# Kernel tuning notes

Hardware: AMD Instinct MI355X
Metric: run time of the kernel (lower is better)

Reference implementation:

```python
import jax, jax.numpy as jnp
import numpy as np

HID = 512
J = 64
NEG = -1e9


def _gru_cell(x, h, Wih, Whh, bih, bhh):
    # PyTorch GRUCell: gates stacked as (r, z, n) along first dim of (3H, in)
    gi = Wih @ x + bih          # (3H,)
    gh = Whh @ h + bhh          # (3H,)
    r = jax.nn.sigmoid(gi[:HID] + gh[:HID])
    z = jax.nn.sigmoid(gi[HID:2 * HID] + gh[HID:2 * HID])
    n = jnp.tanh(gi[2 * HID:] + r * gh[2 * HID:])
    return (1.0 - z) * n + z * h


def setup_inputs() -> dict:
    key = jax.random.key(0)
    ks = jax.random.split(key, 8)
    T = 4096
    state_dim = 2 * J  # input is state[t][1:]
    d = {
        "state": jax.random.normal(ks[0], (T, state_dim + 1), dtype=jnp.float32),
        "h_prev": jnp.zeros((2, HID), dtype=jnp.float32),
        "mask": jax.random.randint(ks[1], (J, J), 0, 2, dtype=jnp.int32),
        "Wih0": jax.random.normal(ks[2], (3 * HID, state_dim), dtype=jnp.float32) * 0.05,
        "Whh0": jax.random.normal(ks[3], (3 * HID, HID), dtype=jnp.float32) * 0.04,
        "bih0": jnp.zeros((3 * HID,), dtype=jnp.float32),
        "bhh0": jnp.zeros((3 * HID,), dtype=jnp.float32),
        "Wih1": jax.random.normal(ks[4], (3 * HID, HID), dtype=jnp.float32) * 0.04,
        "Whh1": jax.random.normal(ks[5], (3 * HID, HID), dtype=jnp.float32) * 0.04,
        "bih1": jnp.zeros((3 * HID,), dtype=jnp.float32),
        "bhh1": jnp.zeros((3 * HID,), dtype=jnp.float32),
        "Wfc": jax.random.normal(ks[6], (J * J, HID), dtype=jnp.float32) * 0.06,
        "bfc": jnp.zeros((J * J,), dtype=jnp.float32),
    }
    return d


def reference(state, h_prev, mask, Wih0, Whh0, bih0, bhh0,
              Wih1, Whh1, bih1, bhh1, Wfc, bfc):
    xs = state[:, 1:]  # drop leading element, matches state[t][1:]

    def step(hs, x_t):
        h0 = _gru_cell(x_t, hs[0], Wih0, Whh0, bih0, bhh0)
        h1 = _gru_cell(h0, hs[1], Wih1, Whh1, bih1, bhh1)
        new = jnp.stack([h0, h1])
        return new, h1

    h_next, h_list = jax.lax.scan(step, h_prev, xs)  # h_list: (T, HID)
    logits = jax.nn.relu(h_list @ Wfc.T + bfc)       # (T, J*J)
    logits = logits.reshape(-1, J, J)
    logits = jnp.where(mask == 0, jnp.float32(NEG), logits)
    return logits, h_next
```

## Files before the change

### kernel.cpp

```cpp
#include <hip/hip_runtime.h>
#include <stdint.h>

#define TSTEPS   4096
#define NEG_VAL  -1000000000.0f
#define NWG_SCAN 96
#define G0WG     32
#define RINGN    32

#define GI0_OFF   0
#define H1_OFF    (TSTEPS*1536*4)
#define RING0_OFF (H1_OFF + TSTEPS*512*4)
#define RING1_OFF (RING0_OFF + RINGN*512*8)
#define ARR_OFF   (RING1_OFF + RINGN*512*8)
#define WS_NEED   ((size_t)ARR_OFF + RINGN*64)

static __device__ __forceinline__ unsigned long long ld_a64(const unsigned long long* p){
  return __hip_atomic_load(p, __ATOMIC_RELAXED, __HIP_MEMORY_SCOPE_AGENT);
}
static __device__ __forceinline__ void st_a64(unsigned long long* p, unsigned long long v){
  __hip_atomic_store(p, v, __ATOMIC_RELAXED, __HIP_MEMORY_SCOPE_AGENT);
}
static __device__ __forceinline__ float sigmoidf_(float x){
  return 1.0f / (1.0f + __expf(-x));
}
static __device__ __forceinline__ float tanhf_(float x){
  float ax = fabsf(x);
  float e  = __expf(-2.0f*ax);
  float t  = (1.0f - e) / (1.0f + e);
  return copysignf(t, x);
}

static __device__ __forceinline__ void spin_to_lds(const unsigned long long* ring, int slot,
                                                   unsigned want, int lane, float* dst,
                                                   long* budget){
  const unsigned long long* bp = ring + (size_t)slot*512 + lane;
  unsigned long long v[8];
  for(;;){
    #pragma unroll
    for (int j=0;j<8;++j) v[j] = ld_a64(bp + j*64);
    bool ok = true;
    #pragma unroll
    for (int j=0;j<8;++j) ok = ok && ((unsigned)(v[j]>>32) == want);
    if (ok) break;
    if (--(*budget) < 0) break;
  }
  #pragma unroll
  for (int j=0;j<8;++j) dst[j*64+lane] = __uint_as_float((unsigned)v[j]);
}

__global__ __launch_bounds__(384,1) void gru_scan(
    const float* __restrict__ gi0,
    const float* __restrict__ hprev,
    const float* __restrict__ Whh0,
    const float* __restrict__ Wih1,
    const float* __restrict__ Whh1,
    const float* __restrict__ bhh0,
    const float* __restrict__ bih1,
    const float* __restrict__ bhh1,
    float* __restrict__ H1hist,
    unsigned long long* ring0,
    unsigned long long* ring1,
    unsigned* arr,
    float* __restrict__ hnext)
{
  const int wg   = blockIdx.x;
  const int tid  = threadIdx.x;
  const int wave = tid >> 6;
  const int lane = tid & 63;

  __shared__ float hbuf0[512];
  __shared__ float hbuf1[512];
  __shared__ float sc[64];

  long budget = (1L<<22);

  if (wg < G0WG) {
    const int ibase = wg*16;
    float w[8][8];
    #pragma unroll
    for (int k=0;k<8;++k){
      const int rid = wave*8+k;
      const int g = rid>>4, il = rid&15;
      const float* wp = Whh0 + ((size_t)(g*512 + ibase + il))*512;
      #pragma unroll
      for (int j=0;j<8;++j) w[k][j] = wp[j*64 + lane];
    }
    float hreg=0.f, br=0.f, bz=0.f, bn_=0.f;
    const int mi = ibase + tid;
    if (tid < 16){
      hreg = hprev[mi];
      br  = bhh0[mi]; bz = bhh0[512+mi]; bn_ = bhh0[1024+mi];
    }
    for (int t=0; t<TSTEPS; ++t){
      float gr=0.f, gz=0.f, gn=0.f;
      if (tid < 16){
        const float* gp = gi0 + (size_t)t*1536 + mi;
        gr = gp[0]; gz = gp[512]; gn = gp[1024];
      }
      if (wave == 0){
        if (t == 0){
          #pragma unroll
          for (int j=0;j<8;++j) hbuf0[j*64+lane] = hprev[j*64+lane];
        } else {
          spin_to_lds(ring0, (t-1)&(RINGN-1), (unsigned)t, lane, hbuf0, &budget);
        }
      }
      if (tid==0 && t>=16){
        unsigned* ap = arr + (size_t)((t-16)&(RINGN-1))*16;
        const unsigned expect = (unsigned)NWG_SCAN * (unsigned)(((t-16)>>5)+1);
        while (__hip_atomic_load(ap, __ATOMIC_RELAXED, __HIP_MEMORY_SCOPE_AGENT) < expect){
          if (--budget < 0) break;
        }
      }
      __syncthreads();
      float hj[8];
      #pragma unroll
      for (int j=0;j<8;++j) hj[j] = hbuf0[j*64+lane];
      float acc[8];
      #pragma unroll
      for (int k=0;k<8;++k){
        float a = 0.f;
        #pragma unroll
        for (int j=0;j<8;++j) a = fmaf(w[k][j], hj[j], a);
        #pragma unroll
        for (int off=32; off; off>>=1) a += __shfl_xor(a, off, 64);
        acc[k] = a;
      }
      if (lane == 0){
        #pragma unroll
        for (int k=0;k<8;++k) sc[wave*8+k] = acc[k];
      }
      __syncthreads();
      if (tid < 16){
        const float ghr = sc[tid]    + br;
        const float ghz = sc[16+tid] + bz;
        const float ghn = sc[32+tid] + bn_;
        const float r = sigmoidf_(gr + ghr);
        const float z = sigmoidf_(gz + ghz);
        const float n = tanhf_(gn + r*ghn);
        const float h = (1.f - z)*n + z*hreg;
        hreg = h;
        st_a64(ring0 + (size_t)(t&(RINGN-1))*512 + mi,
               ((unsigned long long)(unsigned)(t+1)<<32) |
               (unsigned long long)__float_as_uint(h));
        if (t == TSTEPS-1) hnext[mi] = h;
      }
      __syncthreads();
      if (tid == 0){
        __hip_atomic_fetch_add(arr + (size_t)(t&(RINGN-1))*16, 1u,
                               __ATOMIC_RELEASE, __HIP_MEMORY_SCOPE_AGENT);
      }
    }
  } else {
    const int wgl = wg - G0WG;
    const int ibase = wgl*8;
    const bool isA = (wave < 3);
    float w[8][8];
    #pragma unroll
    for (int k=0;k<8;++k){
      const int rid = (isA ? wave : (wave-3))*8 + k;
      const int g = rid>>3, il = rid&7;
      const float* W = isA ? Wih1 : Whh1;
      const float* wp = W + ((size_t)(g*512 + ibase + il))*512;
      #pragma unroll
      for (int j=0;j<8;++j) w[k][j] = wp[j*64 + lane];
    }
    float hreg=0.f, bir=0.f,biz=0.f,bin_=0.f, bhr=0.f,bhz=0.f,bhn=0.f;
    const int mi = ibase + tid;
    if (tid < 8){
      hreg = hprev[512+mi];
      bir = bih1[mi]; biz = bih1[512+mi]; bin_ = bih1[1024+mi];
      bhr = bhh1[mi]; bhz = bhh1[512+mi]; bhn  = bhh1[1024+mi];
    }
    for (int s=0; s<TSTEPS; ++s){
      if (wave == 0){
        spin_to_lds(ring0, s&(RINGN-1), (unsigned)(s+1), lane, hbuf0, &budget);
      } else if (wave == 3){
        if (s == 0){
          #pragma unroll
          for (int j=0;j<8;++j) hbuf1[j*64+lane] = hprev[512 + j*64+lane];
        } else {
          spin_to_lds(ring1, (s-1)&(RINGN-1), (unsigned)s, lane, hbuf1, &budget);
        }
      }
      if (tid==0 && s>=16){
        unsigned* ap = arr + (size_t)((s-16)&(RINGN-1))*16;
        const unsigned expect = (unsigned)NWG_SCAN * (unsigned)(((s-16)>>5)+1);
        while (__hip_atomic_load(ap, __ATOMIC_RELAXED, __HIP_MEMORY_SCOPE_AGENT) < expect){
          if (--budget < 0) break;
        }
      }
      __syncthreads();
      const float* hsrc = isA ? hbuf0 : hbuf1;
      float hj[8];
      #pragma unroll
      for (int j=0;j<8;++j) hj[j] = hsrc[j*64+lane];
      float acc[8];
      #pragma unroll
      for (int k=0;k<8;++k){
        float a = 0.f;
        #pragma unroll
        for (int j=0;j<8;++j) a = fmaf(w[k][j], hj[j], a);
        #pragma unroll
        for (int off=32; off; off>>=1) a += __shfl_xor(a, off, 64);
        acc[k] = a;
      }
      if (lane == 0){
        const int base = isA ? (wave*8) : (24 + (wave-3)*8);
        #pragma unroll
        for (int k=0;k<8;++k) sc[base+k] = acc[k];
      }
      __syncthreads();
      if (tid < 8){
        const float gir = sc[tid]    + bir;
        const float giz = sc[8+tid]  + biz;
        const float gin = sc[16+tid] + bin_;
        const float ghr = sc[24+tid] + bhr;
        const float ghz = sc[32+tid] + bhz;
        const float ghn = sc[40+tid] + bhn;
        const float r = sigmoidf_(gir + ghr);
        const float z = sigmoidf_(giz + ghz);
        const float n = tanhf_(gin + r*ghn);
        const float h = (1.f - z)*n + z*hreg;
        hreg = h;
        st_a64(ring1 + (size_t)(s&(RINGN-1))*512 + mi,
               ((unsigned long long)(unsigned)(s+1)<<32) |
               (unsigned long long)__float_as_uint(h));
        H1hist[(size_t)s*512 + mi] = h;
        if (s == TSTEPS-1) hnext[512+mi] = h;
      }
      __syncthreads();
      if (tid == 0){
        __hip_atomic_fetch_add(arr + (size_t)(s&(RINGN-1))*16, 1u,
                               __ATOMIC_RELEASE, __HIP_MEMORY_SCOPE_AGENT);
      }
    }
  }
}

template<int EPI>
__global__ __launch_bounds__(256) void gemm_nt(
    const float* __restrict__ A, int lda,
    const float* __restrict__ B, int ldb,
    float* __restrict__ C, int ldc,
    const float* __restrict__ bias,
    const int* __restrict__ mask,
    int K)
{
  __shared__ __align__(16) float As[32][68];
  __shared__ __align__(16) float Bs[32][68];
  const int bm = blockIdx.y*64, bn = blockIdx.x*64;
  const int tid = threadIdx.x;
  const int tm = tid>>4, tn = tid&15;
  float acc[4][4] = {};
  const int m0 = tid>>2, kk0 = (tid&3)*8;
  for (int k0=0; k0<K; k0+=32){
    #pragma unroll
    for (int j=0;j<8;++j) As[kk0+j][m0] = A[(size_t)(bm+m0)*lda + k0+kk0+j];
    #pragma unroll
    for (int j=0;j<8;++j) Bs[kk0+j][m0] = B[(size_t)(bn+m0)*ldb + k0+kk0+j];
    __syncthreads();
    #pragma unroll
    for (int kk=0;kk<32;++kk){
      const float4 av = *(const float4*)&As[kk][tm*4];
      const float4 bv = *(const float4*)&Bs[kk][tn*4];
      acc[0][0]=fmaf(av.x,bv.x,acc[0][0]); acc[0][1]=fmaf(av.x,bv.y,acc[0][1]);
      acc[0][2]=fmaf(av.x,bv.z,acc[0][2]); acc[0][3]=fmaf(av.x,bv.w,acc[0][3]);
      acc[1][0]=fmaf(av.y,bv.x,acc[1][0]); acc[1][1]=fmaf(av.y,bv.y,acc[1][1]);
      acc[1][2]=fmaf(av.y,bv.z,acc[1][2]); acc[1][3]=fmaf(av.y,bv.w,acc[1][3]);
      acc[2][0]=fmaf(av.z,bv.x,acc[2][0]); acc[2][1]=fmaf(av.z,bv.y,acc[2][1]);
      acc[2][2]=fmaf(av.z,bv.z,acc[2][2]); acc[2][3]=fmaf(av.z,bv.w,acc[2][3]);
      acc[3][0]=fmaf(av.w,bv.x,acc[3][0]); acc[3][1]=fmaf(av.w,bv.y,acc[3][1]);
      acc[3][2]=fmaf(av.w,bv.z,acc[3][2]); acc[3][3]=fmaf(av.w,bv.w,acc[3][3]);
    }
    __syncthreads();
  }
  #pragma unroll
  for (int i=0;i<4;++i){
    #pragma unroll
    for (int j=0;j<4;++j){
      const int mm = bm + tm*4 + i, cc = bn + tn*4 + j;
      float v = acc[i][j] + bias[cc];
      if (EPI){
        v = fmaxf(v, 0.f);
        if (mask[cc] == 0) v = NEG_VAL;
      }
      C[(size_t)mm*ldc + cc] = v;
    }
  }
}

extern "C" void kernel_launch(void* const* d_in, const int* in_sizes, int n_in,
                              void* d_out, int out_size, void* d_ws, size_t ws_size,
                              hipStream_t stream)
{
  const float* state = (const float*)d_in[0];
  const float* hprev = (const float*)d_in[1];
  const int*   mask  = (const int*)d_in[2];
  const float* Wih0  = (const float*)d_in[3];
  const float* Whh0  = (const float*)d_in[4];
  const float* bih0  = (const float*)d_in[5];
  const float* bhh0  = (const float*)d_in[6];
  const float* Wih1  = (const float*)d_in[7];
  const float* Whh1  = (const float*)d_in[8];
  const float* bih1  = (const float*)d_in[9];
  const float* bhh1  = (const float*)d_in[10];
  const float* Wfc   = (const float*)d_in[11];
  const float* bfc   = (const float*)d_in[12];

  if (ws_size < WS_NEED) return;

  float* out = (float*)d_out;
  char*  ws  = (char*)d_ws;
  float* gi0 = (float*)(ws + GI0_OFF);
  float* H1  = (float*)(ws + H1_OFF);
  unsigned long long* ring0 = (unsigned long long*)(ws + RING0_OFF);
  unsigned long long* ring1 = (unsigned long long*)(ws + RING1_OFF);
  unsigned* arr = (unsigned*)(ws + ARR_OFF);

  (void)hipMemsetAsync(ws + RING0_OFF, 0, (size_t)(WS_NEED - RING0_OFF), stream);

  {
    dim3 grid(1536/64, 4096/64);
    gemm_nt<0><<<grid, 256, 0, stream>>>(state+1, 129, Wih0, 128, gi0, 1536,
                                         bih0, nullptr, 128);
  }

  gru_scan<<<NWG_SCAN, 384, 0, stream>>>(gi0, hprev, Whh0, Wih1, Whh1,
                                         bhh0, bih1, bhh1,
                                         H1, ring0, ring1, arr,
                                         out + (size_t)4096*4096);

  {
    dim3 grid(4096/64, 4096/64);
    gemm_nt<1><<<grid, 256, 0, stream>>>(H1, 512, Wfc, 512, out, 4096,
                                         bfc, mask, 512);
  }
}
```

Before: 12.84 ms.

## Fuse GRU scan with FC GEMM in persistent kernel using fp16 dot2 recurrences

Replaces the scan kernel and the separate FC GEMM with one persistent kernel. Eight workgroups run the layer-0 recurrence, eight run the layer-1 hidden recurrence, and eight compute the layer-1 input projection as a separate pipeline stage. The remaining workgroups take FC GEMM tiles from a ticket counter as H1 rows become ready, so the output GEMM overlaps the serial scan. Weights are held in registers as fp16, and hidden states are exchanged as packed fp16 through small rings with per-slot tags and fdot2, which cuts per-step latency and traffic. The cost is lower precision in the recurrent matvecs and a more complex cross-workgroup synchronisation scheme that can deadlock.

```diff
diff --git a/kernel.cpp b/kernel.cpp
--- a/kernel.cpp
+++ b/kernel.cpp
@@ -1,23 +1,35 @@
 #include <hip/hip_runtime.h>
 #include <stdint.h>
 
-#define TSTEPS   4096
-#define NEG_VAL  -1000000000.0f
-#define NWG_SCAN 96
-#define G0WG     32
-#define RINGN    32
-
-#define GI0_OFF   0
-#define H1_OFF    (TSTEPS*1536*4)
-#define RING0_OFF (H1_OFF + TSTEPS*512*4)
-#define RING1_OFF (RING0_OFF + RINGN*512*8)
-#define ARR_OFF   (RING1_OFF + RINGN*512*8)
-#define WS_NEED   ((size_t)ARR_OFF + RINGN*64)
-
-static __device__ __forceinline__ unsigned long long ld_a64(const unsigned long long* p){
+#define TS 4096
+#define NEG_VAL -1000000000.0f
+
+typedef _Float16 h2 __attribute__((ext_vector_type(2)));
+typedef unsigned long long u64t;
+
+#define GI0_OFF   ((size_t)0)
+#define H1_OFF    ((size_t)TS*1536*4)
+#define R0_OFF    (H1_OFF + (size_t)TS*512*4)
+#define R1_OFF    (R0_OFF + (size_t)16*128*8)
+#define GIR_OFF   (R1_OFF + (size_t)16*128*8)
+#define TAG0_OFF  (GIR_OFF + (size_t)16*1536*4)
+#define TAG1_OFF  (TAG0_OFF + 512)
+#define TAGG_OFF  (TAG1_OFF + 512)
+#define PROGS_OFF (TAGG_OFF + 512)
+#define PROGH_OFF (PROGS_OFF + 128)
+#define TICK_OFF  (PROGH_OFF + 64)
+#define WS_NEED   (TICK_OFF + 64)
+
+static __device__ __forceinline__ u64t ld_a64(const u64t* p){
   return __hip_atomic_load(p, __ATOMIC_RELAXED, __HIP_MEMORY_SCOPE_AGENT);
 }
-static __device__ __forceinline__ void st_a64(unsigned long long* p, unsigned long long v){
+static __device__ __forceinline__ void st_a64(u64t* p, u64t v){
+  __hip_atomic_store(p, v, __ATOMIC_RELAXED, __HIP_MEMORY_SCOPE_AGENT);
+}
+static __device__ __forceinline__ unsigned ld_u32(const unsigned* p){
+  return __hip_atomic_load(p, __ATOMIC_RELAXED, __HIP_MEMORY_SCOPE_AGENT);
+}
+static __device__ __forceinline__ void st_u32(unsigned* p, unsigned v){
   __hip_atomic_store(p, v, __ATOMIC_RELAXED, __HIP_MEMORY_SCOPE_AGENT);
 }
 static __device__ __forceinline__ float sigmoidf_(float x){
@@ -29,223 +41,331 @@
   float t  = (1.0f - e) / (1.0f + e);
   return copysignf(t, x);
 }
-
-static __device__ __forceinline__ void spin_to_lds(const unsigned long long* ring, int slot,
-                                                   unsigned want, int lane, float* dst,
-                                                   long* budget){
-  const unsigned long long* bp = ring + (size_t)slot*512 + lane;
-  unsigned long long v[8];
-  for(;;){
-    #pragma unroll
-    for (int j=0;j<8;++j) v[j] = ld_a64(bp + j*64);
-    bool ok = true;
-    #pragma unroll
-    for (int j=0;j<8;++j) ok = ok && ((unsigned)(v[j]>>32) == want);
-    if (ok) break;
-    if (--(*budget) < 0) break;
-  }
+static __device__ __forceinline__ uint32_t pack2h(float a, float b){
+  _Float16 ha = (_Float16)a, hb = (_Float16)b;
+  unsigned short ua = __builtin_bit_cast(unsigned short, ha);
+  unsigned short ub = __builtin_bit_cast(unsigned short, hb);
+  return (uint32_t)ua | ((uint32_t)ub << 16);
+}
+static __device__ __forceinline__ u64t pk4(float a, float b, float c, float d){
+  return (u64t)pack2h(a,b) | ((u64t)pack2h(c,d) << 32);
+}
+static __device__ __forceinline__ h2 u2h2(uint32_t u){ return __builtin_bit_cast(h2, u); }
+
+template<int CTRL>
+static __device__ __forceinline__ float dppx(float x){
+  return __int_as_float(__builtin_amdgcn_update_dpp(0, __float_as_int(x), CTRL, 0xF, 0xF, true));
+}
+static __device__ __forceinline__ float qsum8(float x){
+  x += dppx<0xB1>(x);
+  x += dppx<0x4E>(x);
+  x += __shfl_xor(x, 4, 64);
+  return x;
+}
+
+#if __has_builtin(__builtin_amdgcn_fdot2)
+#define FDOT2(a,b,c) __builtin_amdgcn_fdot2((a),(b),(c),false)
+#else
+static __device__ __forceinline__ float FDOT2(h2 a, h2 b, float c){
+  return c + (float)a[0]*(float)b[0] + (float)a[1]*(float)b[1];
+}
+#endif
+
+static __device__ __forceinline__ void dot96(const h2 (&w)[96], const u64t* base,
+                                             float& s0, float& s1, float& s2){
+  u64t d[16];
   #pragma unroll
-  for (int j=0;j<8;++j) dst[j*64+lane] = __uint_as_float((unsigned)v[j]);
-}
-
-__global__ __launch_bounds__(384,1) void gru_scan(
-    const float* __restrict__ gi0,
+  for (int i=0;i<16;++i) d[i] = ld_a64(base + i);
+  float a0=0.f, a1=0.f, a2=0.f;
+  #pragma unroll
+  for (int i=0;i<16;++i){
+    h2 lo = u2h2((uint32_t)d[i]);
+    h2 hi = u2h2((uint32_t)(d[i]>>32));
+    a0 = FDOT2(w[2*i],    lo, a0);  a0 = FDOT2(w[2*i+1],    hi, a0);
+    a1 = FDOT2(w[32+2*i], lo, a1);  a1 = FDOT2(w[32+2*i+1], hi, a1);
+    a2 = FDOT2(w[64+2*i], lo, a2);  a2 = FDOT2(w[64+2*i+1], hi, a2);
+  }
+  s0=a0; s1=a1; s2=a2;
+}
+static __device__ __forceinline__ void loadseg(h2* dst, const float* row, int col){
+  const float4* p = (const float4*)(row + col);
+  #pragma unroll
+  for (int k=0;k<16;++k){
+    float4 v = p[k];
+    dst[2*k]   = h2{(_Float16)v.x, (_Float16)v.y};
+    dst[2*k+1] = h2{(_Float16)v.z, (_Float16)v.w};
+  }
+}
+
+__global__ __launch_bounds__(512,1) void actor_fused(
     const float* __restrict__ hprev,
+    const int*   __restrict__ mask,
     const float* __restrict__ Whh0,
+    const float* __restrict__ bhh0,
     const float* __restrict__ Wih1,
     const float* __restrict__ Whh1,
-    const float* __restrict__ bhh0,
     const float* __restrict__ bih1,
     const float* __restrict__ bhh1,
-    float* __restrict__ H1hist,
-    unsigned long long* ring0,
-    unsigned long long* ring1,
-    unsigned* arr,
-    float* __restrict__ hnext)
+    const float* __restrict__ Wfc,
+    const float* __restrict__ bfc,
+    const float* __restrict__ gi0,
+    float* __restrict__ H1,
+    u64t* ring0, u64t* ring1, unsigned* gir,
+    unsigned* tag0, unsigned* tag1, unsigned* tagG,
+    unsigned* progS, unsigned* progH, unsigned* ticket,
+    float* __restrict__ out, float* __restrict__ hnext)
 {
-  const int wg   = blockIdx.x;
-  const int tid  = threadIdx.x;
-  const int wave = tid >> 6;
-  const int lane = tid & 63;
-
-  __shared__ float hbuf0[512];
-  __shared__ float hbuf1[512];
-  __shared__ float sc[64];
-
-  long budget = (1L<<22);
-
-  if (wg < G0WG) {
-    const int ibase = wg*16;
-    float w[8][8];
-    #pragma unroll
-    for (int k=0;k<8;++k){
-      const int rid = wave*8+k;
-      const int g = rid>>4, il = rid&15;
-      const float* wp = Whh0 + ((size_t)(g*512 + ibase + il))*512;
+  const int wg  = blockIdx.x;
+  const int tid = threadIdx.x;
+  __shared__ __align__(16) float lds[6408];
+  long bd = 1L<<21;
+
+  if (wg < 8){
+    const int o = wg*64 + (tid>>3);
+    const int j = tid&7;
+    h2 w[96];
+    loadseg(&w[0],  Whh0 + (size_t)o*512,          64*j);
+    loadseg(&w[32], Whh0 + (size_t)(512+o)*512,    64*j);
+    loadseg(&w[64], Whh0 + (size_t)(1024+o)*512,   64*j);
+    const float br = bhh0[o], bz = bhh0[512+o], bn = bhh0[1024+o];
+    float hreg = hprev[o];
+    if (tid < 16){
+      const float* hp = hprev + wg*64 + 4*tid;
+      st_a64(ring0 + 15*128 + wg*16 + tid, pk4(hp[0],hp[1],hp[2],hp[3]));
+    }
+    asm volatile("s_waitcnt vmcnt(0)" ::: "memory");
+    __syncthreads();
+    if (tid==0) st_u32(tag0 + 15*8 + wg, 1u);
+
+    for (int t=0; t<TS; ++t){
+      if ((t&3)==0 && t>=16){
+        const int need = t-12;
+        for(;;){
+          int mn = 0x7fffffff;
+          #pragma unroll
+          for (int k=0;k<8;++k){ int v=(int)ld_u32(progS+k);    mn = v<mn?v:mn; }
+          #pragma unroll
+          for (int k=16;k<24;++k){ int v=(int)ld_u32(progS+k);  mn = v<mn?v:mn; }
+          if (mn >= need) break;
+          if (--bd < 0) break;
+        }
+      }
+      const float* gp = gi0 + (size_t)t*1536;
+      const float gr = gp[o], gz = gp[512+o], gn = gp[1024+o];
+
+      const int rs = (t-1)&15;
+      const unsigned want = (unsigned)(t+1);
+      { const unsigned* tp = tag0 + rs*8 + j;
+        for(;;){ if (ld_u32(tp) == want) break; if (--bd < 0) break; } }
+
+      float ar, az, an;
+      dot96(w, ring0 + (size_t)rs*128 + 16*j, ar, az, an);
+      ar = qsum8(ar); az = qsum8(az); an = qsum8(an);
+
+      if (tid==4 && (t&3)==0) st_u32(progS + wg, (unsigned)t);
+
+      const float r = sigmoidf_(gr + ar + br);
+      const float z = sigmoidf_(gz + az + bz);
+      const float n = tanhf_(gn + r*(an + bn));
+      const float h = (1.f - z)*n + z*hreg;
+      hreg = h;
+
+      const float hb2 = __shfl_xor(h, 8, 64);
+      const uint32_t p01 = pack2h(h, hb2);
+      const uint32_t p23 = (uint32_t)__shfl_xor((int)p01, 16, 64);
+      if ((tid&31)==0)
+        st_a64(ring0 + (size_t)(t&15)*128 + wg*16 + (tid>>5),
+               (u64t)p01 | ((u64t)p23<<32));
+      if (t==TS-1 && j==0) hnext[o] = h;
+      asm volatile("s_waitcnt vmcnt(0)" ::: "memory");
+      __syncthreads();
+      if (tid==0) st_u32(tag0 + (t&15)*8 + wg, (unsigned)(t+2));
+    }
+  } else if (wg < 16){
+    const int q = wg-8;
+    const int o = q*64 + (tid>>3);
+    const int j = tid&7;
+    h2 w[96];
+    loadseg(&w[0],  Whh1 + (size_t)o*512,          64*j);
+    loadseg(&w[32], Whh1 + (size_t)(512+o)*512,    64*j);
+    loadseg(&w[64], Whh1 + (size_t)(1024+o)*512,   64*j);
+    const float br = bhh1[o], bz = bhh1[512+o], bn = bhh1[1024+o];
+    float hreg = hprev[512+o];
+    if (tid < 16){
+      const float* hp = hprev + 512 + q*64 + 4*tid;
+      st_a64(ring1 + 15*128 + q*16 + tid, pk4(hp[0],hp[1],hp[2],hp[3]));
+    }
+    asm volatile("s_waitcnt vmcnt(0)" ::: "memory");
+    __syncthreads();
+    if (tid==0) st_u32(tag1 + 15*8 + q, 1u);
+
+    for (int s=0; s<TS; ++s){
+      if ((s&3)==0 && s>=16){
+        const int need = s-12;
+        for(;;){
+          int mn = 0x7fffffff;
+          #pragma unroll
+          for (int k=8;k<16;++k){ int v=(int)ld_u32(progS+k); mn = v<mn?v:mn; }
+          if (mn >= need) break;
+          if (--bd < 0) break;
+        }
+      }
+      const int gs = s&15;
+      { const unsigned* tp = tagG + gs*8 + q;
+        const unsigned want = (unsigned)(s+1);
+        for(;;){ if (ld_u32(tp) == want) break; if (--bd < 0) break; } }
+      const float gr = __uint_as_float(ld_u32(gir + gs*1536 + o));
+      const float gz = __uint_as_float(ld_u32(gir + gs*1536 + 512 + o));
+      const float gn = __uint_as_float(ld_u32(gir + gs*1536 + 1024 + o));
+
+      const int rs = (s-1)&15;
+      { const unsigned* tp = tag1 + rs*8 + j;
+        const unsigned want = (unsigned)(s+1);
+        for(;;){ if (ld_u32(tp) == want) break; if (--bd < 0) break; } }
+
+      float ar, az, an;
+      dot96(w, ring1 + (size_t)rs*128 + 16*j, ar, az, an);
+      ar = qsum8(ar); az = qsum8(az); an = qsum8(an);
+
+      if (tid==4 && (s&3)==0) st_u32(progS + wg, (unsigned)s);
+
+      const float r = sigmoidf_(gr + ar + br);
+      const float z = sigmoidf_(gz + az + bz);
+      const float n = tanhf_(gn + r*(an + bn));
+      const float h = (1.f - z)*n + z*hreg;
+      hreg = h;
+
+      if (j==0)
+        __hip_atomic_store(H1 + (size_t)s*512 + o, h,
+                           __ATOMIC_RELAXED, __HIP_MEMORY_SCOPE_AGENT);
+      const float hb2 = __shfl_xor(h, 8, 64);
+      const uint32_t p01 = pack2h(h, hb2);
+      const uint32_t p23 = (uint32_t)__shfl_xor((int)p01, 16, 64);
+      if ((tid&31)==0)
+        st_a64(ring1 + (size_t)(s&15)*128 + q*16 + (tid>>5),
+               (u64t)p01 | ((u64t)p23<<32));
+      if (s==TS-1 && j==0) hnext[512+o] = h;
+      asm volatile("s_waitcnt vmcnt(0)" ::: "memory");
+      __syncthreads();
+      if (tid==0) st_u32(tag1 + (s&15)*8 + q, (unsigned)(s+2));
+      if (tid==8 && (s&15)==15) st_u32(progH + q, (unsigned)(s+1));
+    }
+    __syncthreads();
+    if (tid==8) st_u32(progH + q, (unsigned)TS);
+  } else if (wg < 24){
+    const int hh = wg-16;
+    const int o = hh*64 + (tid>>3);
+    const int j = tid&7;
+    h2 w[96];
+    loadseg(&w[0],  Wih1 + (size_t)o*512,          64*j);
+    loadseg(&w[32], Wih1 + (size_t)(512+o)*512,    64*j);
+    loadseg(&w[64], Wih1 + (size_t)(1024+o)*512,   64*j);
+    const float bia = (j<3) ? bih1[j*512+o] : 0.f;
+
+    for (int s=0; s<TS; ++s){
+      if ((s&3)==0 && s>=16){
+        const int need = s-12;
+        for(;;){
+          int mn = 0x7fffffff;
+          #pragma unroll
+          for (int k=8;k<16;++k){ int v=(int)ld_u32(progS+k); mn = v<mn?v:mn; }
+          if (mn >= need) break;
+          if (--bd < 0) break;
+        }
+      }
+      const int rs = s&15;
+      { const unsigned* tp = tag0 + rs*8 + j;
+        const unsigned want = (unsigned)(s+2);
+        for(;;){ if (ld_u32(tp) == want) break; if (--bd < 0) break; } }
+
+      float g0, g1, g2;
+      dot96(w, ring0 + (size_t)rs*128 + 16*j, g0, g1, g2);
+      g0 = qsum8(g0); g1 = qsum8(g1); g2 = qsum8(g2);
+
+      if (tid==4 && (s&3)==0) st_u32(progS + wg, (unsigned)s);
+
+      if (j < 3){
+        const float gv = ((j==0)?g0 : (j==1)?g1 : g2) + bia;
+        st_u32(gir + rs*1536 + j*512 + o, __float_as_uint(gv));
+      }
+      asm volatile("s_waitcnt vmcnt(0)" ::: "memory");
+      __syncthreads();
+      if (tid==0) st_u32(tagG + rs*8 + hh, (unsigned)(s+1));
+    }
+  } else {
+    float* As = lds;
+    float* Bs = lds + 32*132;
+    int*   comm = (int*)&lds[6404];
+    const int tm = tid>>4, tn = tid&15;
+    const int m0 = tid>>2, kk0a = (tid&3)*8;
+    const int n0 = tid>>3, kk0b = (tid&7)*4;
+    long fcbd = 1L<<24;
+    for(;;){
+      if (tid==0) comm[0] = (int)atomicAdd(ticket, 1u);
+      __syncthreads();
+      const int tau = comm[0];
+      __syncthreads();
+      if (tau >= 2048) break;
+      const int bm = tau>>6, bn = tau&63;
+      if (tid==0){
+        const unsigned need = (unsigned)(bm*128 + 128);
+        for(;;){
+          unsigned mn = 0xffffffffu;
+          #pragma unroll
+          for (int k=0;k<8;++k){ unsigned v = ld_u32(progH+k); mn = v<mn?v:mn; }
+          if (mn >= need) break;
+          __builtin_amdgcn_s_sleep(16);
+          if (--fcbd < 0) break;
+        }
+      }
+      __syncthreads();
+
+      const float* A = H1  + (size_t)bm*128*512;
+      const float* B = Wfc + (size_t)bn*64*512;
+      float acc[4][4] = {};
+      for (int k0=0; k0<512; k0+=32){
+        #pragma unroll
+        for (int jj=0;jj<8;++jj) As[(kk0a+jj)*132 + m0] = A[(size_t)m0*512 + k0+kk0a+jj];
+        #pragma unroll
+        for (int jj=0;jj<4;++jj) Bs[(kk0b+jj)*68  + n0] = B[(size_t)n0*512 + k0+kk0b+jj];
+        __syncthreads();
+        #pragma unroll
+        for (int kk=0;kk<32;++kk){
+          const float4 av = *(const float4*)&As[kk*132 + tm*4];
+          const float4 bv = *(const float4*)&Bs[kk*68  + tn*4];
+          acc[0][0]=fmaf(av.x,bv.x,acc[0][0]); acc[0][1]=fmaf(av.x,bv.y,acc[0][1]);
+          acc[0][2]=fmaf(av.x,bv.z,acc[0][2]); acc[0][3]=fmaf(av.x,bv.w,acc[0][3]);
+          acc[1][0]=fmaf(av.y,bv.x,acc[1][0]); acc[1][1]=fmaf(av.y,bv.y,acc[1][1]);
+          acc[1][2]=fmaf(av.y,bv.z,acc[1][2]); acc[1][3]=fmaf(av.y,bv.w,acc[1][3]);
+          acc[2][0]=fmaf(av.z,bv.x,acc[2][0]); acc[2][1]=fmaf(av.z,bv.y,acc[2][1]);
+          acc[2][2]=fmaf(av.z,bv.z,acc[2][2]); acc[2][3]=fmaf(av.z,bv.w,acc[2][3]);
+          acc[3][0]=fmaf(av.w,bv.x,acc[3][0]); acc[3][1]=fmaf(av.w,bv.y,acc[3][1]);
+          acc[3][2]=fmaf(av.w,bv.z,acc[3][2]); acc[3][3]=fmaf(av.w,bv.w,acc[3][3]);
+        }
+        __syncthreads();
+      }
+      const int cc0 = bn*64 + tn*4;
+      const int mk0 = mask[cc0], mk1 = mask[cc0+1], mk2 = mask[cc0+2], mk3 = mask[cc0+3];
+      const float b0 = bfc[cc0], b1 = bfc[cc0+1], b2 = bfc[cc0+2], b3 = bfc[cc0+3];
       #pragma unroll
-      for (int j=0;j<8;++j) w[k][j] = wp[j*64 + lane];
-    }
-    float hreg=0.f, br=0.f, bz=0.f, bn_=0.f;
-    const int mi = ibase + tid;
-    if (tid < 16){
-      hreg = hprev[mi];
-      br  = bhh0[mi]; bz = bhh0[512+mi]; bn_ = bhh0[1024+mi];
-    }
-    for (int t=0; t<TSTEPS; ++t){
-      float gr=0.f, gz=0.f, gn=0.f;
-      if (tid < 16){
-        const float* gp = gi0 + (size_t)t*1536 + mi;
-        gr = gp[0]; gz = gp[512]; gn = gp[1024];
-      }
-      if (wave == 0){
-        if (t == 0){
-          #pragma unroll
-          for (int j=0;j<8;++j) hbuf0[j*64+lane] = hprev[j*64+lane];
-        } else {
-          spin_to_lds(ring0, (t-1)&(RINGN-1), (unsigned)t, lane, hbuf0, &budget);
-        }
-      }
-      if (tid==0 && t>=16){
-        unsigned* ap = arr + (size_t)((t-16)&(RINGN-1))*16;
-        const unsigned expect = (unsigned)NWG_SCAN * (unsigned)(((t-16)>>5)+1);
-        while (__hip_atomic_load(ap, __ATOMIC_RELAXED, __HIP_MEMORY_SCOPE_AGENT) < expect){
-          if (--budget < 0) break;
-        }
-      }
-      __syncthreads();
-      float hj[8];
-      #pragma unroll
-      for (int j=0;j<8;++j) hj[j] = hbuf0[j*64+lane];
-      float acc[8];
-      #pragma unroll
-      for (int k=0;k<8;++k){
-        float a = 0.f;
-        #pragma unroll
-        for (int j=0;j<8;++j) a = fmaf(w[k][j], hj[j], a);
-        #pragma unroll
-        for (int off=32; off; off>>=1) a += __shfl_xor(a, off, 64);
-        acc[k] = a;
-      }
-      if (lane == 0){
-        #pragma unroll
-        for (int k=0;k<8;++k) sc[wave*8+k] = acc[k];
-      }
-      __syncthreads();
-      if (tid < 16){
-        const float ghr = sc[tid]    + br;
-        const float ghz = sc[16+tid] + bz;
-        const float ghn = sc[32+tid] + bn_;
-        const float r = sigmoidf_(gr + ghr);
-        const float z = sigmoidf_(gz + ghz);
-        const float n = tanhf_(gn + r*ghn);
-        const float h = (1.f - z)*n + z*hreg;
-        hreg = h;
-        st_a64(ring0 + (size_t)(t&(RINGN-1))*512 + mi,
-               ((unsigned long long)(unsigned)(t+1)<<32) |
-               (unsigned long long)__float_as_uint(h));
-        if (t == TSTEPS-1) hnext[mi] = h;
-      }
-      __syncthreads();
-      if (tid == 0){
-        __hip_atomic_fetch_add(arr + (size_t)(t&(RINGN-1))*16, 1u,
-                               __ATOMIC_RELEASE, __HIP_MEMORY_SCOPE_AGENT);
-      }
-    }
-  } else {
-    const int wgl = wg - G0WG;
-    const int ibase = wgl*8;
-    const bool isA = (wave < 3);
-    float w[8][8];
-    #pragma unroll
-    for (int k=0;k<8;++k){
-      const int rid = (isA ? wave : (wave-3))*8 + k;
-      const int g = rid>>3, il = rid&7;
-      const float* W = isA ? Wih1 : Whh1;
-      const float* wp = W + ((size_t)(g*512 + ibase + il))*512;
-      #pragma unroll
-      for (int j=0;j<8;++j) w[k][j] = wp[j*64 + lane];
-    }
-    float hreg=0.f, bir=0.f,biz=0.f,bin_=0.f, bhr=0.f,bhz=0.f,bhn=0.f;
-    const int mi = ibase + tid;
-    if (tid < 8){
-      hreg = hprev[512+mi];
-      bir = bih1[mi]; biz = bih1[512+mi]; bin_ = bih1[1024+mi];
-      bhr = bhh1[mi]; bhz = bhh1[512+mi]; bhn  = bhh1[1024+mi];
-    }
-    for (int s=0; s<TSTEPS; ++s){
-      if (wave == 0){
-        spin_to_lds(ring0, s&(RINGN-1), (unsigned)(s+1), lane, hbuf0, &budget);
-      } else if (wave == 3){
-        if (s == 0){
-          #pragma unroll
-          for (int j=0;j<8;++j) hbuf1[j*64+lane] = hprev[512 + j*64+lane];
-        } else {
-          spin_to_lds(ring1, (s-1)&(RINGN-1), (unsigned)s, lane, hbuf1, &budget);
-        }
-      }
-      if (tid==0 && s>=16){
-        unsigned* ap = arr + (size_t)((s-16)&(RINGN-1))*16;
-        const unsigned expect = (unsigned)NWG_SCAN * (unsigned)(((s-16)>>5)+1);
-        while (__hip_atomic_load(ap, __ATOMIC_RELAXED, __HIP_MEMORY_SCOPE_AGENT) < expect){
-          if (--budget < 0) break;
-        }
-      }
-      __syncthreads();
-      const float* hsrc = isA ? hbuf0 : hbuf1;
-      float hj[8];
-      #pragma unroll
-      for (int j=0;j<8;++j) hj[j] = hsrc[j*64+lane];
-      float acc[8];
-      #pragma unroll
-      for (int k=0;k<8;++k){
-        float a = 0.f;
-        #pragma unroll
-        for (int j=0;j<8;++j) a = fmaf(w[k][j], hj[j], a);
-        #pragma unroll
-        for (int off=32; off; off>>=1) a += __shfl_xor(a, off, 64);
-        acc[k] = a;
-      }
-      if (lane == 0){
-        const int base = isA ? (wave*8) : (24 + (wave-3)*8);
-        #pragma unroll
-        for (int k=0;k<8;++k) sc[base+k] = acc[k];
-      }
-      __syncthreads();
-      if (tid < 8){
-        const float gir = sc[tid]    + bir;
-        const float giz = sc[8+tid]  + biz;
-        const float gin = sc[16+tid] + bin_;
-        const float ghr = sc[24+tid] + bhr;
-        const float ghz = sc[32+tid] + bhz;
-        const float ghn = sc[40+tid] + bhn;
-        const float r = sigmoidf_(gir + ghr);
-        const float z = sigmoidf_(giz + ghz);
-        const float n = tanhf_(gin + r*ghn);
-        const float h = (1.f - z)*n + z*hreg;
-        hreg = h;
-        st_a64(ring1 + (size_t)(s&(RINGN-1))*512 + mi,
-               ((unsigned long long)(unsigned)(s+1)<<32) |
-               (unsigned long long)__float_as_uint(h));
-        H1hist[(size_t)s*512 + mi] = h;
-        if (s == TSTEPS-1) hnext[512+mi] = h;
-      }
-      __syncthreads();
-      if (tid == 0){
-        __hip_atomic_fetch_add(arr + (size_t)(s&(RINGN-1))*16, 1u,
-                               __ATOMIC_RELEASE, __HIP_MEMORY_SCOPE_AGENT);
-      }
-    }
-  }
-}
-
-template<int EPI>
-__global__ __launch_bounds__(256) void gemm_nt(
+      for (int i=0;i<4;++i){
+        const int mm = bm*128 + tm*4 + i;
+        float4 v;
+        v.x = fmaxf(acc[i][0]+b0, 0.f); if (mk0==0) v.x = NEG_VAL;
+        v.y = fmaxf(acc[i][1]+b1, 0.f); if (mk1==0) v.y = NEG_VAL;
+        v.z = fmaxf(acc[i][2]+b2, 0.f); if (mk2==0) v.z = NEG_VAL;
+        v.w = fmaxf(acc[i][3]+b3, 0.f); if (mk3==0) v.w = NEG_VAL;
+        *(float4*)&out[(size_t)mm*4096 + cc0] = v;
+      }
+    }
+  }
+}
+
+__global__ __launch_bounds__(256) void gemm_gi0(
     const float* __restrict__ A, int lda,
     const float* __restrict__ B, int ldb,
     float* __restrict__ C, int ldc,
-    const float* __restrict__ bias,
-    const int* __restrict__ mask,
-    int K)
+    const float* __restrict__ bias, int K)
 {
   __shared__ __align__(16) float As[32][68];
   __shared__ __align__(16) float Bs[32][68];
@@ -280,12 +400,7 @@
     #pragma unroll
     for (int j=0;j<4;++j){
       const int mm = bm + tm*4 + i, cc = bn + tn*4 + j;
-      float v = acc[i][j] + bias[cc];
-      if (EPI){
-        v = fmaxf(v, 0.f);
-        if (mask[cc] == 0) v = NEG_VAL;
-      }
-      C[(size_t)mm*ldc + cc] = v;
+      C[(size_t)mm*ldc + cc] = acc[i][j] + bias[cc];
     }
   }
 }
@@ -314,26 +429,25 @@
   char*  ws  = (char*)d_ws;
   float* gi0 = (float*)(ws + GI0_OFF);
   float* H1  = (float*)(ws + H1_OFF);
-  unsigned long long* ring0 = (unsigned long long*)(ws + RING0_OFF);
-  unsigned long long* ring1 = (unsigned long long*)(ws + RING1_OFF);
-  unsigned* arr = (unsigned*)(ws + ARR_OFF);
-
-  (void)hipMemsetAsync(ws + RING0_OFF, 0, (size_t)(WS_NEED - RING0_OFF), stream);
+  u64t*  ring0 = (u64t*)(ws + R0_OFF);
+  u64t*  ring1 = (u64t*)(ws + R1_OFF);
+  unsigned* gir   = (unsigned*)(ws + GIR_OFF);
+  unsigned* tag0  = (unsigned*)(ws + TAG0_OFF);
+  unsigned* tag1  = (unsigned*)(ws + TAG1_OFF);
+  unsigned* tagG  = (unsigned*)(ws + TAGG_OFF);
+  unsigned* progS = (unsigned*)(ws + PROGS_OFF);
+  unsigned* progH = (unsigned*)(ws + PROGH_OFF);
+  unsigned* tick  = (unsigned*)(ws + TICK_OFF);
+
+  (void)hipMemsetAsync(ws + R0_OFF, 0, (size_t)(WS_NEED - R0_OFF), stream);
 
   {
     dim3 grid(1536/64, 4096/64);
-    gemm_nt<0><<<grid, 256, 0, stream>>>(state+1, 129, Wih0, 128, gi0, 1536,
-                                         bih0, nullptr, 128);
-  }
-
-  gru_scan<<<NWG_SCAN, 384, 0, stream>>>(gi0, hprev, Whh0, Wih1, Whh1,
-                                         bhh0, bih1, bhh1,
-                                         H1, ring0, ring1, arr,
-                                         out + (size_t)4096*4096);
-
-  {
-    dim3 grid(4096/64, 4096/64);
-    gemm_nt<1><<<grid, 256, 0, stream>>>(H1, 512, Wfc, 512, out, 4096,
-                                         bfc, mask, 512);
-  }
-}
+    gemm_gi0<<<grid, 256, 0, stream>>>(state+1, 129, Wih0, 128, gi0, 1536, bih0, 128);
+  }
+
+  actor_fused<<<256, 512, 0, stream>>>(
+      hprev, mask, Whh0, bhh0, Wih1, Whh1, bih1, bhh1, Wfc, bfc,
+      gi0, H1, ring0, ring1, gir, tag0, tag1, tagG, progS, progH, tick,
+      out, out + (size_t)4096*4096);
+}
```

Measured after the change: 21.78 ms. 69.7% more time.
